# Optimization experiments

Hardware: AMD Instinct MI355X
Metric: run time of the kernel (lower is better)

## Reference

```python
import jax, jax.numpy as jnp
import numpy as np

B, C, F, NCLS, NWAY = 512, 1024, 14, 100, 64


def setup_inputs() -> dict:
    key = jax.random.key(0)
    k1, k2, k3 = jax.random.split(key, 3)
    query_features = jax.random.normal(k1, (B, C, F, F), dtype=jnp.float32)
    labels = jax.random.randint(k2, (B,), 0, NWAY)
    prototypes = jax.random.normal(k3, (NCLS, C), dtype=jnp.float32) * 0.05
    indices = jnp.arange(NWAY)  # inverse class mapping: episode class i -> global row
    return {"query_features": query_features, "labels": labels,
            "prototypes": prototypes, "indices": indices, "n_way": NWAY}


def reference(query_features, labels, prototypes, indices, n_way):
    b, c, h, w = query_features.shape
    fsq = h * w
    protos = prototypes[indices]                      # [n_way, C]
    # [B,C,H,W] -> [B*H*W, C], matching permute(0,2,3,1).reshape
    q = jnp.transpose(query_features, (0, 2, 3, 1)).reshape(-1, c)
    # -||q - p||^2 via GEMM trick (same math as expanded pairwise diff)
    qn = jnp.sum(q * q, axis=1, keepdims=True)        # [N,1]
    pn = jnp.sum(protos * protos, axis=1)             # [n_way]
    logits = -(qn + pn[None, :] - 2.0 * (q @ protos.T))  # [N, n_way]
    expanded_labels = jnp.repeat(labels, fsq)         # each pixel inherits image label
    logp = jax.nn.log_softmax(logits, axis=1)
    loss = -jnp.mean(jnp.take_along_axis(logp, expanded_labels[:, None], axis=1))
    return loss
```

## Files before the change

kernel.cpp:

```cpp
#include <hip/hip_runtime.h>
#include <hip/hip_bf16.h>

#define C_DIM 1024
#define HW    196
#define NWAY  64
#define BK    64
#define KSTEPS (C_DIM / BK)
#define LDB   72
#define N_TOT (512 * 196)

typedef short bf16x8 __attribute__((ext_vector_type(8)));
typedef float floatx4 __attribute__((ext_vector_type(4)));
typedef unsigned int u32;

__device__ __forceinline__ unsigned short f2bf(float x) {
    u32 u = __float_as_uint(x);
    u += 0x7fffu + ((u >> 16) & 1u);
    return (unsigned short)(u >> 16);
}

__device__ __forceinline__ bf16x8 pack8(const float v[8]) {
    bf16x8 r;
#pragma unroll
    for (int i = 0; i < 8; ++i) r[i] = (short)f2bf(v[i]);
    return r;
}

__device__ __forceinline__ void gload16(const float* g, float* l) {
    __builtin_amdgcn_global_load_lds(
        (const __attribute__((address_space(1))) u32*)g,
        (__attribute__((address_space(3))) u32*)l, 16, 0, 0);
}

__global__ __launch_bounds__(256, 2) void dfmn_main(
    const float* __restrict__ qf, const int* __restrict__ labels,
    const float* __restrict__ protos, const int* __restrict__ indices,
    float* __restrict__ out)
{
    __shared__ __align__(16) float a_lds[BK * HW];
    __shared__ __align__(16) unsigned short b_lds[NWAY * LDB];
    __shared__ float pn_lds[NWAY];
    __shared__ float wsum[4];

    const int t    = threadIdx.x;
    const int lane = t & 63;
    const int wave = t >> 6;
    const int frm  = lane & 15;
    const int q    = lane >> 4;
    const int b    = blockIdx.x;

    {
        const int cls = t >> 2, part = t & 3;
        const float* prow = protos + (size_t)indices[cls] * C_DIM + part * 256;
        float s = 0.f;
#pragma unroll 4
        for (int i = 0; i < 64; ++i) {
            float4 v = ((const float4*)prow)[i];
            s += v.x * v.x + v.y * v.y + v.z * v.z + v.w * v.w;
        }
        a_lds[t] = s;
    }
    __syncthreads();
    if (t < NWAY) pn_lds[t] = a_lds[4*t] + a_lds[4*t+1] + a_lds[4*t+2] + a_lds[4*t+3];
    __syncthreads();

    const int soct = t & 7;
    const float* pb0 = protos + (size_t)indices[t >> 3] * C_DIM + soct * 8;
    const float* pb1 = protos + (size_t)indices[(t + 256) >> 3] * C_DIM + soct * 8;
    unsigned short* bw0 = &b_lds[(t >> 3) * LDB + soct * 8];
    unsigned short* bw1 = &b_lds[((t + 256) >> 3) * LDB + soct * 8];

    const float* qf_img = qf + (size_t)b * (C_DIM * HW);

    const int mbase = (wave == 0) ? 0 : 4 + 3 * (wave - 1);
    const int mcnt  = (wave == 0) ? 4 : 3;

    floatx4 acc[4][4];
#pragma unroll
    for (int i = 0; i < 4; ++i)
#pragma unroll
        for (int n = 0; n < 4; ++n) acc[i][n] = (floatx4)0.f;

    for (int ks = 0; ks < KSTEPS; ++ks) {
        const int k0 = ks * BK;
        const float* tile = qf_img + (size_t)k0 * HW;

        for (int c = wave; c < 49; c += 4)
            gload16(tile + c * 256 + lane * 4, a_lds + c * 256);

        {
            float4 x0 = *(const float4*)(pb0 + k0);
            float4 x1 = *(const float4*)(pb0 + k0 + 4);
            float v[8] = {x0.x, x0.y, x0.z, x0.w, x1.x, x1.y, x1.z, x1.w};
            *(bf16x8*)bw0 = pack8(v);
            float4 y0 = *(const float4*)(pb1 + k0);
            float4 y1 = *(const float4*)(pb1 + k0 + 4);
            float w[8] = {y0.x, y0.y, y0.z, y0.w, y1.x, y1.y, y1.z, y1.w};
            *(bf16x8*)bw1 = pack8(w);
        }
        __syncthreads();

#pragma unroll
        for (int kk = 0; kk < 2; ++kk) {
            const unsigned short* bb = &b_lds[frm * LDB + kk * 32 + q * 8];
            bf16x8 bv0 = *(const bf16x8*)(bb + 0 * 16 * LDB);
            bf16x8 bv1 = *(const bf16x8*)(bb + 1 * 16 * LDB);
            bf16x8 bv2 = *(const bf16x8*)(bb + 2 * 16 * LDB);
            bf16x8 bv3 = *(const bf16x8*)(bb + 3 * 16 * LDB);
            const float* ak = a_lds + (kk * 32 + q * 8) * HW + frm;
#pragma unroll
            for (int i = 0; i < 4; ++i) {
                if (i < mcnt) {
                    const float* ap = ak + (mbase + i) * 16;
                    float av[8];
#pragma unroll
                    for (int j = 0; j < 8; ++j) av[j] = ap[(size_t)j * HW];
                    bf16x8 a8 = pack8(av);
                    acc[i][0] = __builtin_amdgcn_mfma_f32_16x16x32_bf16(a8, bv0, acc[i][0], 0, 0, 0);
                    acc[i][1] = __builtin_amdgcn_mfma_f32_16x16x32_bf16(a8, bv1, acc[i][1], 0, 0, 0);
                    acc[i][2] = __builtin_amdgcn_mfma_f32_16x16x32_bf16(a8, bv2, acc[i][2], 0, 0, 0);
                    acc[i][3] = __builtin_amdgcn_mfma_f32_16x16x32_bf16(a8, bv3, acc[i][3], 0, 0, 0);
                }
            }
        }
        __syncthreads();
    }

    float pnr[4];
#pragma unroll
    for (int n = 0; n < 4; ++n) pnr[n] = pn_lds[n * 16 + frm];
    const int L   = labels[b];
    const int ntL = L >> 4;
    const int fL  = L & 15;

    float partial = 0.f;
#pragma unroll
    for (int i = 0; i < 4; ++i) {
        if (i < mcnt) {
            const int mt = mbase + i;
#pragma unroll
            for (int r = 0; r < 4; ++r) {
                float l0 = 2.f * acc[i][0][r] - pnr[0];
                float l1 = 2.f * acc[i][1][r] - pnr[1];
                float l2 = 2.f * acc[i][2][r] - pnr[2];
                float l3 = 2.f * acc[i][3][r] - pnr[3];
                float mx = fmaxf(fmaxf(l0, l1), fmaxf(l2, l3));
                mx = fmaxf(mx, __shfl_xor(mx, 1));
                mx = fmaxf(mx, __shfl_xor(mx, 2));
                mx = fmaxf(mx, __shfl_xor(mx, 4));
                mx = fmaxf(mx, __shfl_xor(mx, 8));
                float s = __expf(l0 - mx) + __expf(l1 - mx) + __expf(l2 - mx) + __expf(l3 - mx);
                s += __shfl_xor(s, 1);
                s += __shfl_xor(s, 2);
                s += __shfl_xor(s, 4);
                s += __shfl_xor(s, 8);
                float lse = mx + __logf(s);
                float lL = (ntL == 0) ? l0 : (ntL == 1) ? l1 : (ntL == 2) ? l2 : l3;
                lL = __shfl(lL, (lane & 48) + fL);
                const int px = mt * 16 + q * 4 + r;
                if (px < HW) partial += (lse - lL);
            }
        }
    }
    partial *= (1.f / 16.f) * (1.f / (float)N_TOT);

#pragma unroll
    for (int off = 32; off > 0; off >>= 1) partial += __shfl_down(partial, off, 64);
    if (lane == 0) wsum[wave] = partial;
    __syncthreads();
    if (t == 0) atomicAdd(out, wsum[0] + wsum[1] + wsum[2] + wsum[3]);
}

extern "C" void kernel_launch(void* const* d_in, const int* in_sizes, int n_in,
                              void* d_out, int out_size, void* d_ws, size_t ws_size,
                              hipStream_t stream) {
    const float* qf      = (const float*)d_in[0];
    const int*   labels  = (const int*)d_in[1];
    const float* protos  = (const float*)d_in[2];
    const int*   indices = (const int*)d_in[3];

    hipMemsetAsync(d_out, 0, sizeof(float), stream);
    hipLaunchKernelGGL(dfmn_main, dim3(512), dim3(256), 0, stream,
                       qf, labels, protos, indices, (float*)d_out);
}
```

Baseline: 559.7 us.

## Double-buffer LDS tiles with halved K-step to overlap loads and MFMA

Halves the K tile to 32 and allocates two LDS buffers for the query tile and the bf16 prototype tile. The loop is unrolled by two so the next tile's global-to-LDS loads are issued before the current tile's MFMA work, which is meant to hide global memory latency behind compute. Total LDS stays about the same, but there are twice as many barriers and smaller per-step work.

```diff
diff --git a/kernel.cpp b/kernel.cpp
--- a/kernel.cpp
+++ b/kernel.cpp
@@ -4,9 +4,10 @@
 #define C_DIM 1024
 #define HW    196
 #define NWAY  64
-#define BK    64
+#define BK    32
 #define KSTEPS (C_DIM / BK)
-#define LDB   72
+#define AFLOATS (BK * HW)
+#define LDB   40
 #define N_TOT (512 * 196)
 
 typedef short bf16x8 __attribute__((ext_vector_type(8)));
@@ -32,13 +33,52 @@
         (__attribute__((address_space(3))) u32*)l, 16, 0, 0);
 }
 
+__device__ __forceinline__ void prefetch(const float* qtile, const float* pBk,
+                                         float* abuf, unsigned short* bdst,
+                                         int wave, int lane) {
+    float4 x0 = *(const float4*)(pBk);
+    float4 x1 = *(const float4*)(pBk + 4);
+#pragma unroll
+    for (int i = 0; i < 6; ++i) {
+        const int c = i * 4 + wave;
+        gload16(qtile + c * 256 + lane * 4, abuf + c * 256);
+    }
+    if (wave == 0 && lane < 32)
+        gload16(qtile + 24 * 256 + lane * 4, abuf + 24 * 256);
+    float v[8] = {x0.x, x0.y, x0.z, x0.w, x1.x, x1.y, x1.z, x1.w};
+    *(bf16x8*)bdst = pack8(v);
+}
+
+__device__ __forceinline__ void kcompute(const float* abuf, const unsigned short* bbuf,
+                                         floatx4 acc[4][4], int mbase, int mcnt,
+                                         int frm, int q) {
+    const unsigned short* bb = bbuf + frm * LDB + q * 8;
+    bf16x8 bv[4];
+#pragma unroll
+    for (int n = 0; n < 4; ++n) bv[n] = *(const bf16x8*)(bb + n * 16 * LDB);
+    const float* ak = abuf + (q * 8) * HW + frm;
+#pragma unroll
+    for (int i = 0; i < 4; ++i) {
+        if (i < mcnt) {
+            const float* ap = ak + (mbase + i) * 16;
+            float av[8];
+#pragma unroll
+            for (int j = 0; j < 8; ++j) av[j] = ap[(size_t)j * HW];
+            bf16x8 a8 = pack8(av);
+#pragma unroll
+            for (int n = 0; n < 4; ++n)
+                acc[i][n] = __builtin_amdgcn_mfma_f32_16x16x32_bf16(a8, bv[n], acc[i][n], 0, 0, 0);
+        }
+    }
+}
+
 __global__ __launch_bounds__(256, 2) void dfmn_main(
     const float* __restrict__ qf, const int* __restrict__ labels,
     const float* __restrict__ protos, const int* __restrict__ indices,
     float* __restrict__ out)
 {
-    __shared__ __align__(16) float a_lds[BK * HW];
-    __shared__ __align__(16) unsigned short b_lds[NWAY * LDB];
+    __shared__ __align__(16) float a_lds[2][AFLOATS];
+    __shared__ __align__(16) unsigned short b_lds[2][NWAY * LDB];
     __shared__ float pn_lds[NWAY];
     __shared__ float wsum[4];
 
@@ -58,19 +98,17 @@
             float4 v = ((const float4*)prow)[i];
             s += v.x * v.x + v.y * v.y + v.z * v.z + v.w * v.w;
         }
-        a_lds[t] = s;
+        a_lds[0][t] = s;
     }
     __syncthreads();
-    if (t < NWAY) pn_lds[t] = a_lds[4*t] + a_lds[4*t+1] + a_lds[4*t+2] + a_lds[4*t+3];
+    if (t < NWAY)
+        pn_lds[t] = a_lds[0][4*t] + a_lds[0][4*t+1] + a_lds[0][4*t+2] + a_lds[0][4*t+3];
     __syncthreads();
 
-    const int soct = t & 7;
-    const float* pb0 = protos + (size_t)indices[t >> 3] * C_DIM + soct * 8;
-    const float* pb1 = protos + (size_t)indices[(t + 256) >> 3] * C_DIM + soct * 8;
-    unsigned short* bw0 = &b_lds[(t >> 3) * LDB + soct * 8];
-    unsigned short* bw1 = &b_lds[((t + 256) >> 3) * LDB + soct * 8];
-
     const float* qf_img = qf + (size_t)b * (C_DIM * HW);
+    const float* pB = protos + (size_t)indices[t >> 2] * C_DIM + (t & 3) * 8;
+    unsigned short* bd0 = &b_lds[0][(t >> 2) * LDB + (t & 3) * 8];
+    unsigned short* bd1 = &b_lds[1][(t >> 2) * LDB + (t & 3) * 8];
 
     const int mbase = (wave == 0) ? 0 : 4 + 3 * (wave - 1);
     const int mcnt  = (wave == 0) ? 4 : 3;
@@ -81,48 +119,19 @@
 #pragma unroll
         for (int n = 0; n < 4; ++n) acc[i][n] = (floatx4)0.f;
 
-    for (int ks = 0; ks < KSTEPS; ++ks) {
-        const int k0 = ks * BK;
-        const float* tile = qf_img + (size_t)k0 * HW;
+    prefetch(qf_img, pB, a_lds[0], bd0, wave, lane);
+    __syncthreads();
 
-        for (int c = wave; c < 49; c += 4)
-            gload16(tile + c * 256 + lane * 4, a_lds + c * 256);
-
-        {
-            float4 x0 = *(const float4*)(pb0 + k0);
-            float4 x1 = *(const float4*)(pb0 + k0 + 4);
-            float v[8] = {x0.x, x0.y, x0.z, x0.w, x1.x, x1.y, x1.z, x1.w};
-            *(bf16x8*)bw0 = pack8(v);
-            float4 y0 = *(const float4*)(pb1 + k0);
-            float4 y1 = *(const float4*)(pb1 + k0 + 4);
-            float w[8] = {y0.x, y0.y, y0.z, y0.w, y1.x, y1.y, y1.z, y1.w};
-            *(bf16x8*)bw1 = pack8(w);
-        }
+    for (int ks = 0; ks < KSTEPS; ks += 2) {
+        if (ks + 1 < KSTEPS)
+            prefetch(qf_img + (size_t)(ks + 1) * AFLOATS, pB + (ks + 1) * BK,
+                     a_lds[1], bd1, wave, lane);
+        kcompute(a_lds[0], b_lds[0], acc, mbase, mcnt, frm, q);
         __syncthreads();
-
-#pragma unroll
-        for (int kk = 0; kk < 2; ++kk) {
-            const unsigned short* bb = &b_lds[frm * LDB + kk * 32 + q * 8];
-            bf16x8 bv0 = *(const bf16x8*)(bb + 0 * 16 * LDB);
-            bf16x8 bv1 = *(const bf16x8*)(bb + 1 * 16 * LDB);
-            bf16x8 bv2 = *(const bf16x8*)(bb + 2 * 16 * LDB);
-            bf16x8 bv3 = *(const bf16x8*)(bb + 3 * 16 * LDB);
-            const float* ak = a_lds + (kk * 32 + q * 8) * HW + frm;
-#pragma unroll
-            for (int i = 0; i < 4; ++i) {
-                if (i < mcnt) {
-                    const float* ap = ak + (mbase + i) * 16;
-                    float av[8];
-#pragma unroll
-                    for (int j = 0; j < 8; ++j) av[j] = ap[(size_t)j * HW];
-                    bf16x8 a8 = pack8(av);
-                    acc[i][0] = __builtin_amdgcn_mfma_f32_16x16x32_bf16(a8, bv0, acc[i][0], 0, 0, 0);
-                    acc[i][1] = __builtin_amdgcn_mfma_f32_16x16x32_bf16(a8, bv1, acc[i][1], 0, 0, 0);
-                    acc[i][2] = __builtin_amdgcn_mfma_f32_16x16x32_bf16(a8, bv2, acc[i][2], 0, 0, 0);
-                    acc[i][3] = __builtin_amdgcn_mfma_f32_16x16x32_bf16(a8, bv3, acc[i][3], 0, 0, 0);
-                }
-            }
-        }
+        if (ks + 2 < KSTEPS)
+            prefetch(qf_img + (size_t)(ks + 2) * AFLOATS, pB + (ks + 2) * BK,
+                     a_lds[0], bd0, wave, lane);
+        kcompute(a_lds[1], b_lds[1], acc, mbase, mcnt, frm, q);
         __syncthreads();
     }
 
```

After: 557.1 us. Within noise of the previous version (-0.5%).
